# Performance work log

Hardware: AMD Instinct MI355X
Metric: run time of the kernel (lower is better)

## Reference

```python
import jax, jax.numpy as jnp
import numpy as np

B, S, HID = 2, 1024, 2048
HQ, HKV, HD = 32, 8, 64
ROPE_BASE = 10000.0

def _rope_tables(seq_len, head_dim):
    inv_freq = 1.0 / (ROPE_BASE ** (np.arange(0, head_dim, 2, dtype=np.float32) / head_dim))
    t = np.arange(seq_len, dtype=np.float32)
    freqs = np.outer(t, inv_freq)                      # [S, d/2]
    emb = np.concatenate([freqs, freqs], axis=-1)      # [S, d]
    return jnp.asarray(np.cos(emb)), jnp.asarray(np.sin(emb))

def setup_inputs() -> dict:
    key = jax.random.key(0)
    ks = jax.random.split(key, 5)
    cos, sin = _rope_tables(S, HD)
    return {
        'hidden_states': jax.random.normal(ks[0], (B, S, HID), jnp.float32),
        'cos': cos, 'sin': sin,
        'Wq': jax.random.normal(ks[1], (HID, HID), jnp.float32) * (HID ** -0.5),
        'Wk': jax.random.normal(ks[2], (HID, HKV * HD), jnp.float32) * (HID ** -0.5),
        'Wv': jax.random.normal(ks[3], (HID, HKV * HD), jnp.float32) * (HID ** -0.5),
        'Wo': jax.random.normal(ks[4], (HID, HID), jnp.float32) * (HID ** -0.5),
    }

def _rotate_half(x):
    d = x.shape[-1]
    return jnp.concatenate([-x[..., d // 2:], x[..., :d // 2]], axis=-1)

def reference(hidden_states, cos, sin, Wq, Wk, Wv, Wo):
    b, s, _ = hidden_states.shape
    q = (hidden_states @ Wq).reshape(b, s, HQ, HD)    # [b,s,Hq,d]
    k = (hidden_states @ Wk).reshape(b, s, HKV, HD)   # [b,s,Hkv,d]
    v = (hidden_states @ Wv).reshape(b, s, HKV, HD)
    # RoPE: cos/sin [s,d] broadcast as [s,1,d] over head dim
    c = cos[:, None, :]
    sn = sin[:, None, :]
    q = q * c + _rotate_half(q) * sn
    k = k * c + _rotate_half(k) * sn
    # GQA: expand kv heads to query heads (repeat_kv)
    n_rep = HQ // HKV
    k = jnp.repeat(k, n_rep, axis=2)                  # [b,s,Hq,d]
    v = jnp.repeat(v, n_rep, axis=2)
    scale = HD ** -0.5
    scores = jnp.einsum('bqhd,bkhd->bhqk', q, k) * scale  # [b,Hq,s,s]
    causal = jnp.tril(jnp.ones((s, s), bool))
    scores = jnp.where(causal, scores, jnp.float32(-1e30))
    probs = jax.nn.softmax(scores.astype(jnp.float32), axis=-1).astype(q.dtype)
    out = jnp.einsum('bhqk,bkhd->bqhd', probs, v).reshape(b, s, HID)
    return out @ Wo
```

## Files before the change

kernel.cpp:

```cpp
#include <hip/hip_runtime.h>
#include <math.h>

#define B_   2
#define S_   1024
#define HID_ 2048
#define HQ_  32
#define HKV_ 8
#define HD_  64
#define NQKV 3072

#define PCHUNK 2097152

using short8  = __attribute__((ext_vector_type(8))) short;
using floatx4 = __attribute__((ext_vector_type(4))) float;

__device__ __forceinline__ unsigned short f2bf(float x) {
    unsigned int u = __builtin_bit_cast(unsigned int, x);
    u += 0x7FFFu + ((u >> 16) & 1u);
    return (unsigned short)(u >> 16);
}
__device__ __forceinline__ float bf2f(unsigned short u) {
    return __builtin_bit_cast(float, (unsigned int)u << 16);
}

__device__ __forceinline__ void gl_lds16(const unsigned short* g, unsigned short* l) {
    __builtin_amdgcn_global_load_lds(
        (const __attribute__((address_space(1))) void*)g,
        (__attribute__((address_space(3))) void*)l, 16, 0, 0);
}

__global__ __launch_bounds__(256) void gemm_qkv(const unsigned short* __restrict__ A,
                                                const unsigned short* __restrict__ Bt,
                                                unsigned short* __restrict__ Qp,
                                                unsigned short* __restrict__ KVp) {
    __shared__ __align__(16) unsigned short As[128 * 32];
    __shared__ __align__(16) unsigned short Bs[128 * 32];

    int bid = blockIdx.x;
    int m0, n0, z, Nw, nc0;
    unsigned short* C;
    if (bid < 512) {
        n0 = (bid & 15) * 128; m0 = ((bid >> 4) & 15) * 128; z = bid >> 8;
        C = Qp + (size_t)z * 2048 * 2048; Nw = 2048; nc0 = n0;
    } else {
        bid -= 512;
        n0 = 2048 + (bid & 7) * 128; m0 = ((bid >> 3) & 15) * 128; z = bid >> 7;
        C = KVp + (size_t)z * 2048 * 1024; Nw = 1024; nc0 = n0 - 2048;
    }
    const int kbase = z * 1024;

    const int tid  = threadIdx.x;
    const int w    = tid >> 6;
    const int lane = tid & 63;
    const int col  = lane & 15;
    const int quad = lane >> 4;
    const int wm = (w >> 1) * 64;
    const int wn = (w & 1) * 64;

    const int srow = lane >> 2;
    const int skof = (lane & 3) * 8;
    const unsigned short* Ag = A  + (size_t)(m0 + srow) * HID_ + skof;
    const unsigned short* Bg = Bt + (size_t)(n0 + srow) * HID_ + skof;
    const int rb = w * 16;

    floatx4 acc[4][4] = {};

    for (int k0 = kbase; k0 < kbase + 1024; k0 += 32) {
        gl_lds16(Ag + (size_t)(rb     ) * HID_ + k0, &As[(rb     ) * 32]);
        gl_lds16(Ag + (size_t)(rb + 64) * HID_ + k0, &As[(rb + 64) * 32]);
        gl_lds16(Bg + (size_t)(rb     ) * HID_ + k0, &Bs[(rb     ) * 32]);
        gl_lds16(Bg + (size_t)(rb + 64) * HID_ + k0, &Bs[(rb + 64) * 32]);
        __syncthreads();

        short8 af[4], bfr[4];
#pragma unroll
        for (int i = 0; i < 4; ++i)
            af[i] = *(const short8*)&As[(wm + i * 16 + col) * 32 + quad * 8];
#pragma unroll
        for (int j = 0; j < 4; ++j)
            bfr[j] = *(const short8*)&Bs[(wn + j * 16 + col) * 32 + quad * 8];
#pragma unroll
        for (int i = 0; i < 4; ++i)
#pragma unroll
            for (int j = 0; j < 4; ++j)
                acc[i][j] = __builtin_amdgcn_mfma_f32_16x16x32_bf16(
                    af[i], bfr[j], acc[i][j], 0, 0, 0);
        __syncthreads();
    }

#pragma unroll
    for (int i = 0; i < 4; ++i)
#pragma unroll
        for (int j = 0; j < 4; ++j)
#pragma unroll
            for (int r = 0; r < 4; ++r)
                C[(size_t)(m0 + wm + i * 16 + quad * 4 + r) * Nw
                  + (nc0 + wn + j * 16 + col)] = f2bf(acc[i][j][r]);
}

__global__ __launch_bounds__(256) void gemm_wo(const unsigned short* __restrict__ A,
                                               const unsigned short* __restrict__ Bt,
                                               float* __restrict__ Cf,
                                               unsigned short* __restrict__ Cp1) {
    __shared__ __align__(16) unsigned short As[128 * 32];
    __shared__ __align__(16) unsigned short Bs[128 * 32];

    const int m0 = blockIdx.y * 128;
    const int n0 = blockIdx.x * 128;
    const int z  = blockIdx.z;
    const int kbase = z * 1024;

    const int tid  = threadIdx.x;
    const int w    = tid >> 6;
    const int lane = tid & 63;
    const int col  = lane & 15;
    const int quad = lane >> 4;
    const int wm = (w >> 1) * 64;
    const int wn = (w & 1) * 64;

    const int srow = lane >> 2;
    const int skof = (lane & 3) * 8;
    const unsigned short* Ag = A  + (size_t)(m0 + srow) * HID_ + skof;
    const unsigned short* Bg = Bt + (size_t)(n0 + srow) * HID_ + skof;
    const int rb = w * 16;

    floatx4 acc[4][4] = {};

    for (int k0 = kbase; k0 < kbase + 1024; k0 += 32) {
        gl_lds16(Ag + (size_t)(rb     ) * HID_ + k0, &As[(rb     ) * 32]);
        gl_lds16(Ag + (size_t)(rb + 64) * HID_ + k0, &As[(rb + 64) * 32]);
        gl_lds16(Bg + (size_t)(rb     ) * HID_ + k0, &Bs[(rb     ) * 32]);
        gl_lds16(Bg + (size_t)(rb + 64) * HID_ + k0, &Bs[(rb + 64) * 32]);
        __syncthreads();

        short8 af[4], bfr[4];
#pragma unroll
        for (int i = 0; i < 4; ++i)
            af[i] = *(const short8*)&As[(wm + i * 16 + col) * 32 + quad * 8];
#pragma unroll
        for (int j = 0; j < 4; ++j)
            bfr[j] = *(const short8*)&Bs[(wn + j * 16 + col) * 32 + quad * 8];
#pragma unroll
        for (int i = 0; i < 4; ++i)
#pragma unroll
            for (int j = 0; j < 4; ++j)
                acc[i][j] = __builtin_amdgcn_mfma_f32_16x16x32_bf16(
                    af[i], bfr[j], acc[i][j], 0, 0, 0);
        __syncthreads();
    }

#pragma unroll
    for (int i = 0; i < 4; ++i)
#pragma unroll
        for (int j = 0; j < 4; ++j)
#pragma unroll
            for (int r = 0; r < 4; ++r) {
                size_t off = (size_t)(m0 + wm + i * 16 + quad * 4 + r) * HID_
                           + (n0 + wn + j * 16 + col);
                if (z == 0) Cf[off] = acc[i][j][r];
                else        Cp1[off] = f2bf(acc[i][j][r]);
            }
}

__global__ __launch_bounds__(256) void reduce_wo(float* __restrict__ out,
                                                 const unsigned short* __restrict__ p1) {
    int i4 = (blockIdx.x * 256 + threadIdx.x) * 4;
    float4 o = *(float4*)&out[i4];
    ushort4 p = *(const ushort4*)&p1[i4];
    o.x += bf2f(p.x); o.y += bf2f(p.y); o.z += bf2f(p.z); o.w += bf2f(p.w);
    *(float4*)&out[i4] = o;
}

__global__ __launch_bounds__(256) void convert_x(const float* __restrict__ in,
                                                 unsigned short* __restrict__ out) {
    int tid = blockIdx.x * 256 + threadIdx.x;
    float4 v = *(const float4*)&in[(size_t)tid * 4];
    ushort4 o = {f2bf(v.x), f2bf(v.y), f2bf(v.z), f2bf(v.w)};
    *(ushort4*)&out[(size_t)tid * 4] = o;
}

__global__ __launch_bounds__(256) void transpose_qkv(const float* __restrict__ Wq,
                                                     const float* __restrict__ Wk,
                                                     const float* __restrict__ Wv,
                                                     unsigned short* __restrict__ WcatT) {
    __shared__ float tile[32][33];
    int bid = blockIdx.x;
    const float* W;
    unsigned short* WT;
    int N, tn0, tk0;
    if (bid < 4096) {
        W = Wq; WT = WcatT; N = HID_;
        tn0 = (bid & 63) * 32; tk0 = (bid >> 6) * 32;
    } else if (bid < 5120) {
        bid -= 4096;
        W = Wk; WT = WcatT + (size_t)HID_ * HID_; N = 512;
        tn0 = (bid & 15) * 32; tk0 = (bid >> 4) * 32;
    } else {
        bid -= 5120;
        W = Wv; WT = WcatT + (size_t)(HID_ + 512) * HID_; N = 512;
        tn0 = (bid & 15) * 32; tk0 = (bid >> 4) * 32;
    }
    const int r  = threadIdx.x >> 3;
    const int c4 = (threadIdx.x & 7) * 4;
    float4 v = *(const float4*)&W[(size_t)(tk0 + r) * N + tn0 + c4];
    tile[r][c4 + 0] = v.x;
    tile[r][c4 + 1] = v.y;
    tile[r][c4 + 2] = v.z;
    tile[r][c4 + 3] = v.w;
    __syncthreads();
    ushort4 o = {f2bf(tile[c4 + 0][r]), f2bf(tile[c4 + 1][r]),
                 f2bf(tile[c4 + 2][r]), f2bf(tile[c4 + 3][r])};
    *(ushort4*)&WT[(size_t)(tn0 + r) * HID_ + tk0 + c4] = o;
}

__global__ __launch_bounds__(256) void transpose_wo(const float* __restrict__ Wo,
                                                    unsigned short* __restrict__ WoT) {
    __shared__ float tile[32][33];
    int bid = blockIdx.x;
    const int tn0 = (bid & 63) * 32;
    const int tk0 = (bid >> 6) * 32;
    const int r  = threadIdx.x >> 3;
    const int c4 = (threadIdx.x & 7) * 4;
    float4 v = *(const float4*)&Wo[(size_t)(tk0 + r) * HID_ + tn0 + c4];
    tile[r][c4 + 0] = v.x;
    tile[r][c4 + 1] = v.y;
    tile[r][c4 + 2] = v.z;
    tile[r][c4 + 3] = v.w;
    __syncthreads();
    ushort4 o = {f2bf(tile[c4 + 0][r]), f2bf(tile[c4 + 1][r]),
                 f2bf(tile[c4 + 2][r]), f2bf(tile[c4 + 3][r])};
    *(ushort4*)&WoT[(size_t)(tn0 + r) * HID_ + tk0 + c4] = o;
}

__global__ __launch_bounds__(256) void convert_qkv(const unsigned short* __restrict__ Qp,
                                                   const unsigned short* __restrict__ KVp,
                                                   const float* __restrict__ cosT,
                                                   const float* __restrict__ sinT,
                                                   unsigned short* __restrict__ Qbf,
                                                   unsigned short* __restrict__ Kbf,
                                                   unsigned short* __restrict__ Vt) {
    const size_t QSTR  = (size_t)2048 * 2048;
    const size_t KVSTR = (size_t)2048 * 1024;
    int tid = blockIdx.x * 256 + threadIdx.x;
    const int NQ = B_ * S_ * HQ_ * 32;
    const int NK = B_ * S_ * HKV_ * 32;
    if (tid < NQ) {
        int d = tid & 31;
        int h = (tid >> 5) & (HQ_ - 1);
        int s = (tid >> 10) & (S_ - 1);
        int b = tid >> 20;
        const unsigned short* row = Qp + (size_t)(b * S_ + s) * 2048 + h * HD_;
        float x0 = bf2f(row[d])      + bf2f(row[QSTR + d]);
        float x1 = bf2f(row[d + 32]) + bf2f(row[QSTR + d + 32]);
        float c0 = cosT[s * HD_ + d],      s0 = sinT[s * HD_ + d];
        float c1 = cosT[s * HD_ + d + 32], s1 = sinT[s * HD_ + d + 32];
        unsigned short* orow = Qbf + ((size_t)(b * HQ_ + h) * S_ + s) * HD_;
        orow[d]      = f2bf((x0 * c0 - x1 * s0) * 0.125f);
        orow[d + 32] = f2bf((x1 * c1 + x0 * s1) * 0.125f);
    } else if (tid < NQ + NK) {
        tid -= NQ;
        int d  = tid & 31;
        int kv = (tid >> 5) & (HKV_ - 1);
        int s  = (tid >> 8) & (S_ - 1);
        int b  = tid >> 18;
        const unsigned short* row = KVp + (size_t)(b * S_ + s) * 1024 + kv * HD_;
        float x0 = bf2f(row[d])      + bf2f(row[KVSTR + d]);
        float x1 = bf2f(row[d + 32]) + bf2f(row[KVSTR + d + 32]);
        float c0 = cosT[s * HD_ + d],      s0 = sinT[s * HD_ + d];
        float c1 = cosT[s * HD_ + d + 32], s1 = sinT[s * HD_ + d + 32];
        unsigned short* orow = Kbf + ((size_t)(b * HKV_ + kv) * S_ + s) * HD_;
        orow[d]      = f2bf(x0 * c0 - x1 * s0);
        orow[d + 32] = f2bf(x1 * c1 + x0 * s1);
    } else {
        tid -= NQ + NK;
        int s4 = tid & 255;
        int d  = (tid >> 8) & (HD_ - 1);
        int kv = (tid >> 14) & (HKV_ - 1);
        int b  = tid >> 17;
        int s  = s4 * 4;
        const unsigned short* base =
            KVp + ((size_t)(b * S_ + s)) * 1024 + 512 + kv * HD_ + d;
        ushort4 o;
#pragma unroll
        for (int j = 0; j < 4; ++j) {
            float v = bf2f(base[(size_t)j * 1024]) +
                      bf2f(base[KVSTR + (size_t)j * 1024]);
            ((unsigned short*)&o)[j] = f2bf(v);
        }
        *(ushort4*)&Vt[((size_t)(b * HKV_ + kv) * HD_ + d) * S_ + s] = o;
    }
}

__global__ __launch_bounds__(256) void attn_mfma(const unsigned short* __restrict__ Qbf,
                                                 const unsigned short* __restrict__ Kbf,
                                                 const unsigned short* __restrict__ Vt,
                                                 unsigned short* __restrict__ Ctx,
                                                 float* __restrict__ PO,
                                                 float* __restrict__ ML) {
    const int x  = blockIdx.x;
    const int kv = blockIdx.y;
    const int b  = blockIdx.z;

    int tq, chunk, it0, it1;
    if (x < 32) {
        tq = 16 + (x >> 1); chunk = x & 1;
        const int ns = (32 * tq + 95) >> 6;
        const int hh = ns >> 1;
        it0 = chunk ? hh : 0;
        it1 = chunk ? ns : hh;
    } else {
        tq = 47 - x; chunk = -1;
        it0 = 0;
        it1 = (32 * tq + 95) >> 6;
    }

    const int w    = threadIdx.x >> 6;
    const int lane = threadIdx.x & 63;
    const int col  = lane & 15;
    const int quad = lane >> 4;

    const int h   = kv * 4 + w;
    const int bh  = b * HQ_ + h;
    const int bkv = b * HKV_ + kv;
    const int qw  = 32 * tq;

    __shared__ __align__(16) unsigned short sK[2][64 * 64];
    __shared__ __align__(16) unsigned short sV[2][64 * 64];
    __shared__ __align__(16) unsigned short sP[4][32 * 72];
    unsigned short* myP = sP[w];

    short8 bq[2][2];
#pragma unroll
    for (int u = 0; u < 2; ++u) {
        const unsigned short* qrow = Qbf + ((size_t)bh * S_ + qw + 16 * u + col) * HD_;
        bq[u][0] = *(const short8*)&qrow[quad * 8];
        bq[u][1] = *(const short8*)&qrow[32 + quad * 8];
    }

    const unsigned short* Kbase = Kbf + (size_t)bkv * S_ * HD_;
    const unsigned short* Vbase = Vt  + (size_t)bkv * HD_ * S_;

    const int sr  = lane >> 3;
    const int ssl = (lane & 7) ^ sr;
    const int r0  = 16 * w;

    floatx4 acc[2][4] = {};
    float m_i[2] = {-1e30f, -1e30f};
    float l_i[2] = {0.f, 0.f};

    {
        const int kb = it0 * 64;
#pragma unroll
        for (int c = 0; c < 2; ++c) {
            const int row = r0 + 8 * c + sr;
            gl_lds16(Kbase + (size_t)(kb + row) * HD_ + ssl * 8, &sK[0][(r0 + 8 * c) * 64]);
            gl_lds16(Vbase + (size_t)row * S_ + kb + ssl * 8,    &sV[0][(r0 + 8 * c) * 64]);
        }
    }
    __syncthreads();

    int cur = 0;
    for (int it = it0; it < it1; ++it) {
        const int k0 = it * 64;

        if (it + 1 < it1) {
            const int kn = k0 + 64;
#pragma unroll
            for (int c = 0; c < 2; ++c) {
                const int row = r0 + 8 * c + sr;
                gl_lds16(Kbase + (size_t)(kn + row) * HD_ + ssl * 8,
                         &sK[cur ^ 1][(r0 + 8 * c) * 64]);
                gl_lds16(Vbase + (size_t)row * S_ + kn + ssl * 8,
                         &sV[cur ^ 1][(r0 + 8 * c) * 64]);
            }
        }

        floatx4 sc[2][4];
        __builtin_amdgcn_s_setprio(1);
#pragma unroll
        for (int tt = 0; tt < 4; ++tt) {
            const int krow = 16 * tt + col;
            const unsigned short* kr = &sK[cur][krow * 64];
            short8 ak0 = *(const short8*)&kr[((quad    ) ^ (krow & 7)) * 8];
            short8 ak1 = *(const short8*)&kr[((quad + 4) ^ (krow & 7)) * 8];
#pragma unroll
            for (int u = 0; u < 2; ++u) {
                floatx4 z = {0.f, 0.f, 0.f, 0.f};
                z = __builtin_amdgcn_mfma_f32_16x16x32_bf16(ak0, bq[u][0], z, 0, 0, 0);
                z = __builtin_amdgcn_mfma_f32_16x16x32_bf16(ak1, bq[u][1], z, 0, 0, 0);
                sc[u][tt] = z;
            }
        }
        __builtin_amdgcn_s_setprio(0);

#pragma unroll
        for (int u = 0; u < 2; ++u) {
            const int qbase = qw + 16 * u;
            const int myq   = qbase + col;
            if (k0 + 63 > qbase) {
#pragma unroll
                for (int tt = 0; tt < 4; ++tt)
#pragma unroll
                    for (int r = 0; r < 4; ++r)
                        if (k0 + 16 * tt + quad * 4 + r > myq) sc[u][tt][r] = -1e30f;
            }
            float vmax = sc[u][0][0];
#pragma unroll
            for (int tt = 0; tt < 4; ++tt)
#pragma unroll
                for (int r = 0; r < 4; ++r)
                    vmax = fmaxf(vmax, sc[u][tt][r]);
            vmax = fmaxf(vmax, __shfl_xor(vmax, 16, 64));
            vmax = fmaxf(vmax, __shfl_xor(vmax, 32, 64));
            const float mnew  = fmaxf(m_i[u], vmax);
            const float alpha = __expf(m_i[u] - mnew);
            m_i[u] = mnew;
            float lsum = 0.f;
#pragma unroll
            for (int tt = 0; tt < 4; ++tt) {
                float p0 = __expf(sc[u][tt][0] - mnew);
                float p1 = __expf(sc[u][tt][1] - mnew);
                float p2 = __expf(sc[u][tt][2] - mnew);
                float p3 = __expf(sc[u][tt][3] - mnew);
                lsum += (p0 + p1) + (p2 + p3);
                ushort4 pk = {f2bf(p0), f2bf(p1), f2bf(p2), f2bf(p3)};
                *(ushort4*)&myP[(16 * u + col) * 72 + 16 * tt + quad * 4] = pk;
            }
            lsum += __shfl_xor(lsum, 16, 64);
            lsum += __shfl_xor(lsum, 32, 64);
            l_i[u] = l_i[u] * alpha + lsum;
            float a_r[4];
#pragma unroll
            for (int r = 0; r < 4; ++r)
                a_r[r] = __shfl(alpha, quad * 4 + r, 64);
#pragma unroll
            for (int nt = 0; nt < 4; ++nt)
#pragma unroll
                for (int r = 0; r < 4; ++r)
                    acc[u][nt][r] *= a_r[r];
        }

        short8 pa[2][2];
#pragma unroll
        for (int u = 0; u < 2; ++u) {
            pa[u][0] = *(const short8*)&myP[(16 * u + col) * 72 + quad * 8];
            pa[u][1] = *(const short8*)&myP[(16 * u + col) * 72 + 32 + quad * 8];
        }
        __builtin_amdgcn_s_setprio(1);
#pragma unroll
        for (int nt = 0; nt < 4; ++nt) {
            const int vrow = 16 * nt + col;
            const unsigned short* vr = &sV[cur][vrow * 64];
            short8 vb0 = *(const short8*)&vr[((quad    ) ^ (vrow & 7)) * 8];
            short8 vb1 = *(const short8*)&vr[((quad + 4) ^ (vrow & 7)) * 8];
#pragma unroll
            for (int u = 0; u < 2; ++u) {
                acc[u][nt] = __builtin_amdgcn_mfma_f32_16x16x32_bf16(pa[u][0], vb0, acc[u][nt], 0, 0, 0);
                acc[u][nt] = __builtin_amdgcn_mfma_f32_16x16x32_bf16(pa[u][1], vb1, acc[u][nt], 0, 0, 0);
            }
        }
        __builtin_amdgcn_s_setprio(0);

        __syncthreads();
        cur ^= 1;
    }

    if (chunk < 0) {
#pragma unroll
        for (int u = 0; u < 2; ++u) {
            const float invl = 1.0f / l_i[u];
            float inv_r[4];
#pragma unroll
            for (int r = 0; r < 4; ++r)
                inv_r[r] = __shfl(invl, quad * 4 + r, 64);
#pragma unroll
            for (int nt = 0; nt < 4; ++nt)
#pragma unroll
                for (int r = 0; r < 4; ++r)
                    Ctx[(size_t)(b * S_ + qw + 16 * u + quad * 4 + r) * HID_
                        + h * HD_ + nt * 16 + col] = f2bf(acc[u][nt][r] * inv_r[r]);
        }
    } else {
        const int ts = tq - 16;
        const int base_row = (((b * 8 + kv) * 16 + ts) * 4 + w) * 32;
        float* POc = PO + (size_t)chunk * PCHUNK;
#pragma unroll
        for (int u = 0; u < 2; ++u)
#pragma unroll
            for (int nt = 0; nt < 4; ++nt)
#pragma unroll
                for (int r = 0; r < 4; ++r)
                    POc[(size_t)(base_row + 16 * u + quad * 4 + r) * 64
                        + nt * 16 + col] = acc[u][nt][r];
        if (quad == 0) {
#pragma unroll
            for (int u = 0; u < 2; ++u) {
                const int rr = chunk * 32768 + base_row + 16 * u + col;
                ML[rr * 2 + 0] = m_i[u];
                ML[rr * 2 + 1] = l_i[u];
            }
        }
    }
}

__global__ __launch_bounds__(256) void merge_attn(const float* __restrict__ PO,
                                                  const float* __restrict__ ML,
                                                  unsigned short* __restrict__ Ctx) {
    const int tid = blockIdx.x * 256 + threadIdx.x;
    const int i4  = tid * 4;
    const int row = i4 >> 6;
    const int d0  = i4 & 63;

    const float m0 = ML[row * 2 + 0];
    const float l0 = ML[row * 2 + 1];
    const float m1 = ML[(32768 + row) * 2 + 0];
    const float l1 = ML[(32768 + row) * 2 + 1];
    const float mf = fmaxf(m0, m1);
    const float s0 = __expf(m0 - mf);
    const float s1 = __expf(m1 - mf);
    const float inv = 1.0f / (l0 * s0 + l1 * s1);

    float4 o0 = *(const float4*)&PO[(size_t)row * 64 + d0];
    float4 o1 = *(const float4*)&PO[(size_t)PCHUNK + (size_t)row * 64 + d0];

    const int q  = row & 31;
    const int hh = (row >> 5) & 3;
    const int ts = (row >> 7) & 15;
    const int kv = (row >> 11) & 7;
    const int b  = row >> 14;
    const int q_abs = 512 + ts * 32 + q;
    const int h_abs = kv * 4 + hh;

    ushort4 o;
    o.x = f2bf((o0.x * s0 + o1.x * s1) * inv);
    o.y = f2bf((o0.y * s0 + o1.y * s1) * inv);
    o.z = f2bf((o0.z * s0 + o1.z * s1) * inv);
    o.w = f2bf((o0.w * s0 + o1.w * s1) * inv);
    *(ushort4*)&Ctx[((size_t)(b * S_ + q_abs)) * HID_ + h_abs * HD_ + d0] = o;
}

extern "C" void kernel_launch(void* const* d_in, const int* in_sizes, int n_in,
                              void* d_out, int out_size, void* d_ws, size_t ws_size,
                              hipStream_t stream) {
    const float* X    = (const float*)d_in[0];
    const float* cosT = (const float*)d_in[1];
    const float* sinT = (const float*)d_in[2];
    const float* Wq   = (const float*)d_in[3];
    const float* Wk   = (const float*)d_in[4];
    const float* Wv   = (const float*)d_in[5];
    const float* Wo   = (const float*)d_in[6];

    const int M = B_ * S_;
    const size_t MB = 1024u * 1024u;

    char* ws = (char*)d_ws;
    unsigned short* Xbf   = (unsigned short*)(ws);
    unsigned short* Qbf   = (unsigned short*)(ws);
    unsigned short* WcatT = (unsigned short*)(ws + 8 * MB);
    unsigned short* Kbf   = (unsigned short*)(ws + 8 * MB);
    unsigned short* Vt    = (unsigned short*)(ws + 10 * MB);
    float*          MLb   = (float*)(ws + 12 * MB);
    unsigned short* WoT   = (unsigned short*)(ws + 12 * MB);
    unsigned short* KVp   = (unsigned short*)(ws + 20 * MB);
    unsigned short* Ctxbf = (unsigned short*)(ws + 20 * MB);
    unsigned short* Wop1  = (unsigned short*)(ws);
    unsigned short* Qp    = (unsigned short*)d_out;
    float*          PO    = (float*)d_out;
    float* out = (float*)d_out;

    convert_x<<<(M * HID_ / 4) / 256, 256, 0, stream>>>(X, Xbf);

    transpose_qkv<<<6144, 256, 0, stream>>>(Wq, Wk, Wv, WcatT);

    gemm_qkv<<<768, 256, 0, stream>>>(Xbf, WcatT, Qp, KVp);

    {
        int total = B_ * S_ * HQ_ * 32 + B_ * S_ * HKV_ * 32
                  + B_ * HKV_ * HD_ * (S_ / 4);
        convert_qkv<<<total / 256, 256, 0, stream>>>(Qp, KVp, cosT, sinT,
                                                     Qbf, Kbf, Vt);
    }

    attn_mfma<<<dim3(48, HKV_, B_), 256, 0, stream>>>(Qbf, Kbf, Vt, Ctxbf,
                                                      PO, MLb);

    merge_attn<<<2048, 256, 0, stream>>>(PO, MLb, Ctxbf);

    transpose_wo<<<4096, 256, 0, stream>>>(Wo, WoT);

    gemm_wo<<<dim3(16, 16, 2), 256, 0, stream>>>(Ctxbf, WoT, out, Wop1);

    reduce_wo<<<(M * HID_ / 4) / 256, 256, 0, stream>>>(out, Wop1);
}
```

Before: 246.1 us.

## Transpose PV MFMA, skip lazy rescale, shrink swizzled P buffer

The P·V MFMA now takes its operands in swapped order, so each lane's accumulator holds a query row across consecutive head-dim columns. That removes the per-row alpha shuffles and allows vectorized Ctx and PO stores. The online softmax skips the max update and accumulator rescale when the new block max stays within 8 of the running max, a wave-uniform test. P is staged in a smaller XOR-swizzled per-u LDS tile that is reused across u, and it is read back right after being written. Deferring the rescale lets exponents grow up to e^8 before renormalisation, which trades a small precision margin for fewer multiplies.

```diff
diff --git a/kernel.cpp b/kernel.cpp
--- a/kernel.cpp
+++ b/kernel.cpp
@@ -326,7 +326,7 @@
 
     __shared__ __align__(16) unsigned short sK[2][64 * 64];
     __shared__ __align__(16) unsigned short sV[2][64 * 64];
-    __shared__ __align__(16) unsigned short sP[4][32 * 72];
+    __shared__ __align__(16) unsigned short sP[4][16 * 64];
     unsigned short* myP = sP[w];
 
     short8 bq[2][2];
@@ -393,6 +393,7 @@
         }
         __builtin_amdgcn_s_setprio(0);
 
+        short8 pa[2][2];
 #pragma unroll
         for (int u = 0; u < 2; ++u) {
             const int qbase = qw + 16 * u;
@@ -412,40 +413,41 @@
                     vmax = fmaxf(vmax, sc[u][tt][r]);
             vmax = fmaxf(vmax, __shfl_xor(vmax, 16, 64));
             vmax = fmaxf(vmax, __shfl_xor(vmax, 32, 64));
-            const float mnew  = fmaxf(m_i[u], vmax);
-            const float alpha = __expf(m_i[u] - mnew);
-            m_i[u] = mnew;
+
+            if (!__all(vmax <= m_i[u] + 8.0f)) {
+                const float mnew  = fmaxf(m_i[u], vmax);
+                const float alpha = __expf(m_i[u] - mnew);
+                m_i[u] = mnew;
+                l_i[u] *= alpha;
+#pragma unroll
+                for (int nt = 0; nt < 4; ++nt)
+#pragma unroll
+                    for (int r = 0; r < 4; ++r)
+                        acc[u][nt][r] *= alpha;
+            }
+            const float mu = m_i[u];
+
             float lsum = 0.f;
 #pragma unroll
             for (int tt = 0; tt < 4; ++tt) {
-                float p0 = __expf(sc[u][tt][0] - mnew);
-                float p1 = __expf(sc[u][tt][1] - mnew);
-                float p2 = __expf(sc[u][tt][2] - mnew);
-                float p3 = __expf(sc[u][tt][3] - mnew);
+                float p0 = __expf(sc[u][tt][0] - mu);
+                float p1 = __expf(sc[u][tt][1] - mu);
+                float p2 = __expf(sc[u][tt][2] - mu);
+                float p3 = __expf(sc[u][tt][3] - mu);
                 lsum += (p0 + p1) + (p2 + p3);
                 ushort4 pk = {f2bf(p0), f2bf(p1), f2bf(p2), f2bf(p3)};
-                *(ushort4*)&myP[(16 * u + col) * 72 + 16 * tt + quad * 4] = pk;
+                *(ushort4*)&myP[col * 64
+                                + ((((4 * tt + quad) >> 1) ^ (col & 7)) << 3)
+                                + (quad & 1) * 4] = pk;
             }
             lsum += __shfl_xor(lsum, 16, 64);
             lsum += __shfl_xor(lsum, 32, 64);
-            l_i[u] = l_i[u] * alpha + lsum;
-            float a_r[4];
-#pragma unroll
-            for (int r = 0; r < 4; ++r)
-                a_r[r] = __shfl(alpha, quad * 4 + r, 64);
-#pragma unroll
-            for (int nt = 0; nt < 4; ++nt)
-#pragma unroll
-                for (int r = 0; r < 4; ++r)
-                    acc[u][nt][r] *= a_r[r];
-        }
-
-        short8 pa[2][2];
-#pragma unroll
-        for (int u = 0; u < 2; ++u) {
-            pa[u][0] = *(const short8*)&myP[(16 * u + col) * 72 + quad * 8];
-            pa[u][1] = *(const short8*)&myP[(16 * u + col) * 72 + 32 + quad * 8];
-        }
+            l_i[u] += lsum;
+
+            pa[u][0] = *(const short8*)&myP[col * 64 + (((quad    ) ^ (col & 7)) << 3)];
+            pa[u][1] = *(const short8*)&myP[col * 64 + (((4 + quad) ^ (col & 7)) << 3)];
+        }
+
         __builtin_amdgcn_s_setprio(1);
 #pragma unroll
         for (int nt = 0; nt < 4; ++nt) {
@@ -455,8 +457,8 @@
             short8 vb1 = *(const short8*)&vr[((quad + 4) ^ (vrow & 7)) * 8];
 #pragma unroll
             for (int u = 0; u < 2; ++u) {
-                acc[u][nt] = __builtin_amdgcn_mfma_f32_16x16x32_bf16(pa[u][0], vb0, acc[u][nt], 0, 0, 0);
-                acc[u][nt] = __builtin_amdgcn_mfma_f32_16x16x32_bf16(pa[u][1], vb1, acc[u][nt], 0, 0, 0);
+                acc[u][nt] = __builtin_amdgcn_mfma_f32_16x16x32_bf16(vb0, pa[u][0], acc[u][nt], 0, 0, 0);
+                acc[u][nt] = __builtin_amdgcn_mfma_f32_16x16x32_bf16(vb1, pa[u][1], acc[u][nt], 0, 0, 0);
             }
         }
         __builtin_amdgcn_s_setprio(0);
@@ -469,32 +471,26 @@
 #pragma unroll
         for (int u = 0; u < 2; ++u) {
             const float invl = 1.0f / l_i[u];
-            float inv_r[4];
-#pragma unroll
-            for (int r = 0; r < 4; ++r)
-                inv_r[r] = __shfl(invl, quad * 4 + r, 64);
-#pragma unroll
-            for (int nt = 0; nt < 4; ++nt)
-#pragma unroll
-                for (int r = 0; r < 4; ++r)
-                    Ctx[(size_t)(b * S_ + qw + 16 * u + quad * 4 + r) * HID_
-                        + h * HD_ + nt * 16 + col] = f2bf(acc[u][nt][r] * inv_r[r]);
+            unsigned short* crow =
+                Ctx + (size_t)(b * S_ + qw + 16 * u + col) * HID_ + h * HD_;
+#pragma unroll
+            for (int nt = 0; nt < 4; ++nt) {
+                ushort4 o = {f2bf(acc[u][nt][0] * invl), f2bf(acc[u][nt][1] * invl),
+                             f2bf(acc[u][nt][2] * invl), f2bf(acc[u][nt][3] * invl)};
+                *(ushort4*)&crow[nt * 16 + quad * 4] = o;
+            }
         }
     } else {
         const int ts = tq - 16;
         const int base_row = (((b * 8 + kv) * 16 + ts) * 4 + w) * 32;
         float* POc = PO + (size_t)chunk * PCHUNK;
 #pragma unroll
-        for (int u = 0; u < 2; ++u)
+        for (int u = 0; u < 2; ++u) {
+            float* prow = &POc[(size_t)(base_row + 16 * u + col) * 64];
 #pragma unroll
             for (int nt = 0; nt < 4; ++nt)
-#pragma unroll
-                for (int r = 0; r < 4; ++r)
-                    POc[(size_t)(base_row + 16 * u + quad * 4 + r) * 64
-                        + nt * 16 + col] = acc[u][nt][r];
-        if (quad == 0) {
-#pragma unroll
-            for (int u = 0; u < 2; ++u) {
+                *(floatx4*)&prow[nt * 16 + quad * 4] = acc[u][nt];
+            if (quad == 0) {
                 const int rr = chunk * 32768 + base_row + 16 * u + col;
                 ML[rr * 2 + 0] = m_i[u];
                 ML[rr * 2 + 1] = l_i[u];
```

Result: no change. 246.6 us (+0.2%).
